# Optimization experiments

Measured on AMD Instinct MI355X. Metric: run time of the kernel, lower is better.

## Reference

```python
import jax, jax.numpy as jnp
import numpy as np

TOPK = 32
NUM_PT = 8192
NUM_KP = 8
HW = 19200


def _conv3(x, w, b):
    # x: [1, C, N], w: [O, C, 3] -> [1, O, N] (padding=1)
    y = jax.lax.conv_general_dilated(x, w, (1,), [(1, 1)],
                                     dimension_numbers=('NCH', 'OIH', 'NCH'))
    return y + b[None, :, None]


def setup_inputs() -> dict:
    key = jax.random.key(0)
    ks = jax.random.split(key, 64)

    def p(i, *shape):
        return (jax.random.normal(ks[i], shape, dtype=jnp.float32) * 0.05)

    inp = {
        'seg': jax.random.uniform(ks[0], (1, NUM_PT), dtype=jnp.float32),
        'img': jax.random.normal(ks[1], (1, 32, HW), dtype=jnp.float32),
        'cloud': jax.random.normal(ks[2], (1, NUM_PT, 3), dtype=jnp.float32),
        't': jax.random.normal(ks[3], (1, 3), dtype=jnp.float32),
        'choose': jax.random.randint(ks[4], (1, 1, NUM_PT), 0, HW),
        # Pseudo3DConv params (all 1x1 conv1d == channel matmul)
        'pconv1_w': p(5, 64, 3),    'pconv1_b': p(6, 64),
        'pconv2_w': p(7, 128, 64),  'pconv2_b': p(8, 128),
        'conv1_w': p(9, 64, 32),    'conv1_b': p(10, 64),
        'conv2_w': p(11, 128, 64),  'conv2_b': p(12, 128),
        'psconv1_w': p(13, 256, 128), 'psconv1_b': p(14, 256),
        'psconv2_w': p(15, 128, 256), 'psconv2_b': p(16, 128),
        'final_w': p(17, 128, 416), 'final_b': p(18, 128),
        # heads
        'seg1_w': p(19, 64, 128, 3), 'seg1_b': p(20, 64),
        'seg2_w': p(21, 32, 64),     'seg2_b': p(22, 32),
        'seg3_w': p(23, 1, 32),      'seg3_b': p(24, 1),
        'dis1_w': p(25, 64, 128, 3), 'dis1_b': p(26, 64),
        'dis2_w': p(27, 32, 64),     'dis2_b': p(28, 32),
        'dis3_w': p(29, 1, 32),      'dis3_b': p(30, 1),
        'lin1_w': p(31, 90, 128),    'lin1_b': p(32, 90),
        'lin2_w': p(33, 64, 90),     'lin2_b': p(34, 64),
        'lin3_w': p(35, 3 * NUM_KP, 64), 'lin3_b': p(36, 3 * NUM_KP),
    }
    return inp


def reference(seg, img, cloud, t, choose,
              pconv1_w, pconv1_b, pconv2_w, pconv2_b,
              conv1_w, conv1_b, conv2_w, conv2_b,
              psconv1_w, psconv1_b, psconv2_w, psconv2_b,
              final_w, final_b,
              seg1_w, seg1_b, seg2_w, seg2_b, seg3_w, seg3_b,
              dis1_w, dis1_b, dis2_w, dis2_b, dis3_w, dis3_b,
              lin1_w, lin1_b, lin2_w, lin2_b, lin3_w, lin3_b):
    lrelu = jax.nn.leaky_relu  # slope 0.01, same as torch default
    N = NUM_PT

    # gather per-point image features at chosen pixels: [N, 32]
    feat = jnp.take(img[0], choose[0, 0], axis=1).T
    c = cloud[0]  # [N, 3]

    # ---- KNN (self included, as in knn_cuda) ----
    d2 = jnp.sum((c[:, None, :] - c[None, :, :]) ** 2, axis=-1)  # [N, N]
    _, idx = jax.lax.top_k(-d2, TOPK)  # [N, K] nearest neighbors

    # ---- point-feature MLP (pconv1 -> lrelu -> pconv2) ----
    pf = lrelu(c @ pconv1_w.T + pconv1_b) @ pconv2_w.T + pconv2_b  # [N, 128]

    # ---- vectorized per-point neighbor gather + MLP + weighted maxpool ----
    nf = feat[idx]    # [N, K, 32]
    npf = pf[idx]     # [N, K, 128]
    npos = c[idx]     # [N, K, 3]
    w = jax.nn.softmax(-jnp.linalg.norm(c[:, None, :] - npos, axis=-1), axis=1)  # [N, K]

    f = lrelu(nf @ conv1_w.T + conv1_b) @ conv2_w.T + conv2_b          # [N, K, 128]
    fp = lrelu(npf @ psconv1_w.T + psconv1_b) @ psconv2_w.T + psconv2_b  # [N, K, 128]
    f = jnp.max(f * w[..., None], axis=1)    # [N, 128]
    fp = jnp.max(fp * w[..., None], axis=1)  # [N, 128]

    # final2 = [fp | img_feat], final1 = [f | cloud_feat] -> cat -> [N, 416]
    final = jnp.concatenate([fp, feat, f, pf], axis=1)
    fused = lrelu(final) @ final_w.T + final_b  # [N, 128]
    fused = fused.T[None]  # [1, 128, N]

    def pw(x, w_, b_):  # 1x1 conv1d on [1, C, N]
        return jnp.einsum('oc,bcn->bon', w_, x) + b_[None, :, None]

    # segmentation head
    h = lrelu(_conv3(fused, seg1_w, seg1_b))
    seg_pre = pw(lrelu(pw(h, seg2_w, seg2_b)), seg3_w, seg3_b).reshape(1, N)

    # distance-to-center weighting (norm along coord dim, softmax over points)
    dis_center = jax.nn.softmax(
        jnp.linalg.norm(cloud - (-t)[:, None, :], axis=2), axis=1)  # [1, N]

    # distance head (on unweighted fused features, matching torch op order)
    h = lrelu(_conv3(fused, dis1_w, dis1_b))
    dis_pre = pw(lrelu(pw(h, dis2_w, dis2_b)), dis3_w, dis3_b).reshape(1, N)

    # weight fused features by center distance and segmentation, sum-pool
    fused = fused * dis_center[:, None, :] * seg[:, None, :]
    g = jnp.sum(fused, axis=2)  # [1, 128]

    kp = lrelu(g @ lin1_w.T + lin1_b)
    kp = lrelu(kp @ lin2_w.T + lin2_b)
    keypoints = (kp @ lin3_w.T + lin3_b).reshape(1, NUM_KP, 3)
    return keypoints, dis_pre, dis_center, seg_pre
```

## Files before the change

kernel.cpp:

```cpp
#include <hip/hip_runtime.h>
#include <math.h>

#define NPT 8192
#define HWIMG 19200
#define KCAP 128

using short8 = __attribute__((ext_vector_type(8))) short;
using short4v = __attribute__((ext_vector_type(4))) short;
using f32x4  = __attribute__((ext_vector_type(4))) float;

__device__ __forceinline__ float lrelu(float x) { return x > 0.f ? x : 0.01f * x; }
__device__ __forceinline__ unsigned short f2bf(float v) {
  unsigned u = __float_as_uint(v);
  return (unsigned short)((u + 0x7fffu + ((u >> 16) & 1u)) >> 16);
}
__device__ __forceinline__ float bf2f(unsigned short h) {
  return __uint_as_float(((unsigned)h) << 16);
}
__device__ __forceinline__ void split2(float v, unsigned short& h, unsigned short& l) {
  h = f2bf(v);
  l = f2bf(v - bf2f(h));
}
__device__ __forceinline__ void mfma3(f32x4& acc, short8 ah, short8 al, short8 wh, short8 wl) {
  acc = __builtin_amdgcn_mfma_f32_16x16x32_bf16(ah, wh, acc, 0, 0, 0);
  acc = __builtin_amdgcn_mfma_f32_16x16x32_bf16(al, wh, acc, 0, 0, 0);
  acc = __builtin_amdgcn_mfma_f32_16x16x32_bf16(ah, wl, acc, 0, 0, 0);
}

__device__ __forceinline__ int swz(int o, int k, int Kc) {
  return ((((o >> 4) * Kc + (k >> 5)) << 6) + (((k >> 3) & 3) << 4) + (o & 15)) * 8 + (k & 7);
}

#define OFF_PCONV2  0
#define OFF_CONV1   8192
#define OFF_CONV2   10240
#define OFF_PSCONV1 18432
#define OFF_PSCONV2 51200
#define OFF_FINAL   83968
#define OFF_W3      137216
#define OFF_W2P     186368

#define S_C4    NPT
#define S_G     129
#define S_BIASC 128
#define S_B2C   64
#define S_FEAT  (NPT*32)
#define S_W3    49152
#define S_W2P   8192
#define S_WSPL  OFF_W3
#define PREP_TOTAL (S_C4 + S_G + S_BIASC + S_B2C + S_FEAT + S_W3 + S_W2P + S_WSPL)
__global__ void k_prep(const float* __restrict__ cloud, const int* __restrict__ choose,
                       const float* __restrict__ img,
                       const float* __restrict__ seg1_w, const float* __restrict__ dis1_w,
                       const float* __restrict__ seg1_b, const float* __restrict__ dis1_b,
                       const float* __restrict__ seg2_w, const float* __restrict__ dis2_w,
                       const float* __restrict__ seg2_b, const float* __restrict__ dis2_b,
                       const float* __restrict__ pconv2_w, const float* __restrict__ conv1_w,
                       const float* __restrict__ conv2_w, const float* __restrict__ psconv1_w,
                       const float* __restrict__ psconv2_w, const float* __restrict__ final_w,
                       float* __restrict__ c4, float* __restrict__ g,
                       float* __restrict__ biasc, float* __restrict__ bias2c,
                       float* __restrict__ feat,
                       unsigned short* __restrict__ feat_h, unsigned short* __restrict__ feat_l,
                       unsigned short* __restrict__ Wh, unsigned short* __restrict__ Wl) {
  int j = blockIdx.x * blockDim.x + threadIdx.x;
  if (j < S_C4) {
    float x = cloud[j*3+0], y = cloud[j*3+1], z = cloud[j*3+2];
    float4 v; v.x = x; v.y = y; v.z = z; v.w = x*x + y*y + z*z;
    ((float4*)c4)[j] = v;
    return;
  }
  j -= S_C4;
  if (j < S_G) { g[j] = 0.f; return; }
  j -= S_G;
  if (j < S_BIASC) { biasc[j] = (j < 64) ? seg1_b[j] : dis1_b[j-64]; return; }
  j -= S_BIASC;
  if (j < S_B2C) { bias2c[j] = (j < 32) ? seg2_b[j] : dis2_b[j-32]; return; }
  j -= S_B2C;
  if (j < S_FEAT) {
    int n = j >> 5, ch = j & 31;
    float v = img[ch*HWIMG + choose[n]];
    feat[j] = v;
    unsigned short hh, ll; split2(v, hh, ll);
    int d = swz(n, ch, 1);
    feat_h[d] = hh; feat_l[d] = ll;
    return;
  }
  j -= S_FEAT;
  if (j < S_W3) {
    int h = j / 24576, r = j - h*24576, o = r / 384, k = r - o*384;
    int t = k >> 7, c = k & 127;
    float v = (h ? dis1_w : seg1_w)[o*384 + c*3 + t];
    unsigned short hh, ll; split2(v, hh, ll);
    int d = OFF_W3 + swz(h*64 + o, k, 12);
    Wh[d] = hh; Wl[d] = ll;
    return;
  }
  j -= S_W3;
  if (j < S_W2P) {
    int o = j >> 7, c = j & 127;
    float v = 0.f;
    if (o < 32) { if (c < 64) v = seg2_w[o*64 + c]; }
    else        { if (c >= 64) v = dis2_w[(o-32)*64 + (c-64)]; }
    unsigned short hh, ll; split2(v, hh, ll);
    int d = OFF_W2P + swz(o, c, 4);
    Wh[d] = hh; Wl[d] = ll;
    return;
  }
  j -= S_W2P;
  if (j < S_WSPL) {
    float v; int d;
    if (j < OFF_CONV1) {
      int o = j >> 6, k = j & 63;
      v = pconv2_w[j]; d = OFF_PCONV2 + swz(o, k, 2);
    } else if (j < OFF_CONV2) {
      int jj = j - OFF_CONV1, o = jj >> 5, k = jj & 31;
      v = conv1_w[jj]; d = OFF_CONV1 + swz(o, k, 1);
    } else if (j < OFF_PSCONV1) {
      int jj = j - OFF_CONV2, o = jj >> 6, k = jj & 63;
      v = conv2_w[jj]; d = OFF_CONV2 + swz(o, k, 2);
    } else if (j < OFF_PSCONV2) {
      int jj = j - OFF_PSCONV1, o = jj >> 7, k = jj & 127;
      v = psconv1_w[jj]; d = OFF_PSCONV1 + swz(o, k, 4);
    } else if (j < OFF_FINAL) {
      int jj = j - OFF_PSCONV2, o = jj >> 8, k = jj & 255;
      v = psconv2_w[jj]; d = OFF_PSCONV2 + swz(o, k, 8);
    } else {
      int jj = j - OFF_FINAL, o = jj / 416, k = jj - o*416;
      v = final_w[jj]; d = OFF_FINAL + swz(o, k, 13);
    }
    unsigned short hh, ll; split2(v, hh, ll);
    Wh[d] = hh; Wl[d] = ll;
  }
}

__device__ __forceinline__ unsigned bsort32u(unsigned key, int lane) {
#pragma unroll
  for (int k = 2; k <= 64; k <<= 1) {
#pragma unroll
    for (int j = k >> 1; j > 0; j >>= 1) {
      unsigned o = __shfl_xor(key, j, 64);
      bool keepmin = (((lane & j) == 0) == ((lane & k) == 0));
      key = ((o < key) == keepmin) ? o : key;
    }
  }
  return key;
}
__device__ __forceinline__ unsigned long long bsort64(unsigned long long key, int lane) {
#pragma unroll
  for (int k = 2; k <= 64; k <<= 1) {
#pragma unroll
    for (int j = k >> 1; j > 0; j >>= 1) {
      unsigned long long o = __shfl_xor(key, j, 64);
      bool keepmin = (((lane & j) == 0) == ((lane & k) == 0));
      bool omin = o < key;
      key = (omin == keepmin) ? o : key;
    }
  }
  return key;
}
__device__ __forceinline__ unsigned long long bmerge64(unsigned long long key, int lane) {
#pragma unroll
  for (int j = 32; j > 0; j >>= 1) {
    unsigned long long o = __shfl_xor(key, j, 64);
    bool keepmin = ((lane & j) == 0);
    bool omin = o < key;
    key = (omin == keepmin) ? o : key;
  }
  return key;
}

#define MEGA_GRID 3073
__global__ __launch_bounds__(256) void k_mega(const float4* __restrict__ c4,
                                              int* __restrict__ idxo, float* __restrict__ wo,
                                              const float* __restrict__ cloud,
                                              const float* __restrict__ tvec,
                                              float* __restrict__ dc,
                                              const float* __restrict__ pconv1_w, const float* __restrict__ pconv1_b,
                                              const float* __restrict__ pconv2_b, const float* __restrict__ psconv1_b,
                                              const float* __restrict__ psconv2_b,
                                              const unsigned short* __restrict__ feat_h,
                                              const unsigned short* __restrict__ feat_l,
                                              const float* __restrict__ conv1_b, const float* __restrict__ conv2_b,
                                              const unsigned short* __restrict__ Wh,
                                              const unsigned short* __restrict__ Wl,
                                              float* __restrict__ pf, float* __restrict__ Yfp,
                                              float* __restrict__ Yf) {
  __shared__ __align__(16) char smem[16384];
  int tid = threadIdx.x, lane = tid & 63, w = tid >> 6;
  int mr = lane & 15, q = lane >> 4;
  if (blockIdx.x > 2048) {
    unsigned short* sh_h = (unsigned short*)smem;
    unsigned short* sh_l = (unsigned short*)(smem + 8192);
    int cb = blockIdx.x - 2049;
    if (cb < 512) {
      int m0 = cb * 16;
      float4 cp = c4[m0 + mr];
      short8 ah0, al0, ah1, al1;
#pragma unroll
      for (int j = 0; j < 8; ++j) {
        int c0 = q*8 + j, c1 = 32 + q*8 + j;
        float v0 = lrelu(fmaf(cp.x, pconv1_w[c0*3+0], fmaf(cp.y, pconv1_w[c0*3+1],
                          fmaf(cp.z, pconv1_w[c0*3+2], pconv1_b[c0]))));
        float v1 = lrelu(fmaf(cp.x, pconv1_w[c1*3+0], fmaf(cp.y, pconv1_w[c1*3+1],
                          fmaf(cp.z, pconv1_w[c1*3+2], pconv1_b[c1]))));
        unsigned short hh, ll;
        split2(v0, hh, ll); ah0[j] = (short)hh; al0[j] = (short)ll;
        split2(v1, hh, ll); ah1[j] = (short)hh; al1[j] = (short)ll;
      }
      f32x4 acc[2];
#pragma unroll
      for (int t = 0; t < 2; ++t) { f32x4 z = {0.f,0.f,0.f,0.f}; acc[t] = z; }
      const unsigned short* W2h = Wh + OFF_PCONV2;
      const unsigned short* W2l = Wl + OFF_PCONV2;
#pragma unroll
      for (int tt = 0; tt < 2; ++tt) {
        int t1 = 2*w + tt;
        int w0 = ((t1*2 + 0)*64 + lane)*8, w1 = ((t1*2 + 1)*64 + lane)*8;
        mfma3(acc[tt], ah0, al0, *(const short8*)(W2h + w0), *(const short8*)(W2l + w0));
        mfma3(acc[tt], ah1, al1, *(const short8*)(W2h + w1), *(const short8*)(W2l + w1));
      }
#pragma unroll
      for (int tt = 0; tt < 2; ++tt) {
        int t1 = 2*w + tt, n = t1*16 + mr;
        float b = pconv2_b[n];
        int ks2 = t1 >> 1, q2 = (t1 & 1)*2 + (mr >> 3), jd = mr & 7;
#pragma unroll
        for (int r = 0; r < 4; ++r) {
          int row = q*4 + r;
          float v = acc[tt][r] + b;
          pf[(size_t)(m0+row)*128 + n] = v;
          unsigned short hh, ll; split2(v, hh, ll);
          int p = ((ks2*16 + row)*4 + q2)*8 + jd;
          sh_h[p] = hh; sh_l[p] = ll;
        }
      }
      __syncthreads();
      f32x4 acc3[2];
#pragma unroll
      for (int t = 0; t < 2; ++t) { f32x4 z = {0.f,0.f,0.f,0.f}; acc3[t] = z; }
      const unsigned short* W3h = Wh + OFF_PSCONV1;
      const unsigned short* W3l = Wl + OFF_PSCONV1;
      const unsigned short* W4h = Wh + OFF_PSCONV2;
      const unsigned short* W4l = Wl + OFF_PSCONV2;
#pragma unroll
      for (int h = 0; h < 2; ++h) {
        f32x4 acc2[2];
#pragma unroll
        for (int t = 0; t < 2; ++t) { f32x4 z = {0.f,0.f,0.f,0.f}; acc2[t] = z; }
#pragma unroll
        for (int ks = 0; ks < 4; ++ks) {
          int ap = ((ks*16 + mr)*4 + q)*8;
          short8 ah = *(const short8*)&sh_h[ap];
          short8 al = *(const short8*)&sh_l[ap];
#pragma unroll
          for (int tt = 0; tt < 2; ++tt) {
            int ts = h*8 + 2*w + tt;
            int wb = ((ts*4 + ks)*64 + lane)*8;
            mfma3(acc2[tt], ah, al, *(const short8*)(W3h + wb), *(const short8*)(W3l + wb));
          }
        }
#pragma unroll
        for (int tt = 0; tt < 2; ++tt) {
          int tl = 2*w + tt;
          int n = h*128 + tl*16 + mr;
          float b = psconv1_b[n];
          int ks3 = tl >> 1, q3 = (tl & 1)*2 + (mr >> 3), jd = mr & 7;
#pragma unroll
          for (int r = 0; r < 4; ++r) {
            int row = q*4 + r;
            float v = lrelu(acc2[tt][r] + b);
            unsigned short hh, ll; split2(v, hh, ll);
            int p = 2048 + ((ks3*16 + row)*4 + q3)*8 + jd;
            sh_h[p] = hh; sh_l[p] = ll;
          }
        }
        __syncthreads();
#pragma unroll
        for (int ks = 0; ks < 4; ++ks) {
          int ap = 2048 + ((ks*16 + mr)*4 + q)*8;
          short8 ah = *(const short8*)&sh_h[ap];
          short8 al = *(const short8*)&sh_l[ap];
#pragma unroll
          for (int tt = 0; tt < 2; ++tt) {
            int wb = (((2*w+tt)*8 + h*4 + ks)*64 + lane)*8;
            mfma3(acc3[tt], ah, al, *(const short8*)(W4h + wb), *(const short8*)(W4l + wb));
          }
        }
        __syncthreads();
      }
#pragma unroll
      for (int tt = 0; tt < 2; ++tt) {
        int n = (2*w+tt)*16 + mr;
        float b = psconv2_b[n];
#pragma unroll
        for (int r = 0; r < 4; ++r)
          Yfp[(size_t)(m0 + q*4 + r)*128 + n] = acc3[tt][r] + b;
      }
    } else {
      int m0 = (cb - 512) * 16;
      int ab = ((m0 >> 4)*64 + lane)*8;
      short8 ah = *(const short8*)(feat_h + ab);
      short8 al = *(const short8*)(feat_l + ab);
      f32x4 acc = {0.f,0.f,0.f,0.f};
      const unsigned short* W1h = Wh + OFF_CONV1;
      const unsigned short* W1l = Wl + OFF_CONV1;
      {
        int wb = (w*64 + lane)*8;
        mfma3(acc, ah, al, *(const short8*)(W1h + wb), *(const short8*)(W1l + wb));
      }
      {
        int n = w*16 + mr;
        float b = conv1_b[n];
        int ks2 = n >> 5, q2 = (n >> 3) & 3, jd = mr & 7;
#pragma unroll
        for (int r = 0; r < 4; ++r) {
          int row = q*4 + r;
          float v = lrelu(acc[r] + b);
          unsigned short hh, ll; split2(v, hh, ll);
          int p = ((ks2*16 + row)*4 + q2)*8 + jd;
          sh_h[p] = hh; sh_l[p] = ll;
        }
      }
      __syncthreads();
      f32x4 acc2[2];
#pragma unroll
      for (int t = 0; t < 2; ++t) { f32x4 z = {0.f,0.f,0.f,0.f}; acc2[t] = z; }
      const unsigned short* W2h = Wh + OFF_CONV2;
      const unsigned short* W2l = Wl + OFF_CONV2;
#pragma unroll
      for (int ks = 0; ks < 2; ++ks) {
        int ap = ((ks*16 + mr)*4 + q)*8;
        short8 a2 = *(const short8*)&sh_h[ap];
        short8 a2l = *(const short8*)&sh_l[ap];
#pragma unroll
        for (int tt = 0; tt < 2; ++tt) {
          int wb = (((2*w+tt)*2 + ks)*64 + lane)*8;
          mfma3(acc2[tt], a2, a2l, *(const short8*)(W2h + wb), *(const short8*)(W2l + wb));
        }
      }
#pragma unroll
      for (int tt = 0; tt < 2; ++tt) {
        int n = (2*w+tt)*16 + mr;
        float b = conv2_b[n];
#pragma unroll
        for (int r = 0; r < 4; ++r)
          Yf[(size_t)(m0 + q*4 + r)*128 + n] = acc2[tt][r] + b;
      }
    }
    return;
  }
  if (blockIdx.x == 2048) {
    float* sred = (float*)smem;
    float tx = tvec[0], ty = tvec[1], tz = tvec[2];
    float v[32];
    float m = -INFINITY;
#pragma unroll
    for (int i2 = 0; i2 < 32; ++i2) {
      int n = i2*256 + tid;
      float ax = cloud[n*3+0] + tx, ay = cloud[n*3+1] + ty, az = cloud[n*3+2] + tz;
      v[i2] = sqrtf(ax*ax + ay*ay + az*az);
      m = fmaxf(m, v[i2]);
    }
#pragma unroll
    for (int o = 1; o < 64; o <<= 1) m = fmaxf(m, __shfl_xor(m, o, 64));
    if (lane == 0) sred[w] = m;
    __syncthreads();
    m = fmaxf(fmaxf(sred[0], sred[1]), fmaxf(sred[2], sred[3]));
    __syncthreads();
    float s = 0.f;
#pragma unroll
    for (int i2 = 0; i2 < 32; ++i2) { v[i2] = expf(v[i2] - m); s += v[i2]; }
#pragma unroll
    for (int o = 1; o < 64; o <<= 1) s += __shfl_xor(s, o, 64);
    if (lane == 0) sred[w] = s;
    __syncthreads();
    s = sred[0] + sred[1] + sred[2] + sred[3];
#pragma unroll
    for (int i2 = 0; i2 < 32; ++i2) dc[i2*256 + tid] = v[i2] / s;
    return;
  }
  float (*smin)[256] = (float(*)[256])smem;
  float* sTv = (float*)(smem + 4096);
  int*   scnt = (int*)(smem + 4112);
  float (*sd)[KCAP] = (float(*)[KCAP])(smem + 4128);
  int   (*sj)[KCAP] = (int(*)[KCAP])(smem + 6176);
  int q0 = blockIdx.x * 4;
  float4 p0 = c4[q0], p1 = c4[q0+1], p2 = c4[q0+2], p3 = c4[q0+3];
  float p0x = -2.f*p0.x, p0y = -2.f*p0.y, p0z = -2.f*p0.z;
  float p1x = -2.f*p1.x, p1y = -2.f*p1.y, p1z = -2.f*p1.z;
  float p2x = -2.f*p2.x, p2y = -2.f*p2.y, p2z = -2.f*p2.z;
  float p3x = -2.f*p3.x, p3y = -2.f*p3.y, p3z = -2.f*p3.z;
#define DDOT(PX,PY,PZ,PW,CJ) fmaf(PX,(CJ).x, fmaf(PY,(CJ).y, fmaf(PZ,(CJ).z, PW + (CJ).w)))
  float m0 = INFINITY, m1 = INFINITY, m2 = INFINITY, m3 = INFINITY;
  for (int t = 0; t < 32; ++t) {
    float4 cj = c4[t*256 + tid];
    m0 = fminf(m0, DDOT(p0x,p0y,p0z,p0.w,cj));
    m1 = fminf(m1, DDOT(p1x,p1y,p1z,p1.w,cj));
    m2 = fminf(m2, DDOT(p2x,p2y,p2z,p2.w,cj));
    m3 = fminf(m3, DDOT(p3x,p3y,p3z,p3.w,cj));
  }
  smin[0][tid] = m0; smin[1][tid] = m1; smin[2][tid] = m2; smin[3][tid] = m3;
  if (tid < 4) scnt[tid] = 0;
  __syncthreads();
  {
    float4 vv = *(const float4*)&smin[w][lane*4];
    float m4 = fmaxf(fminf(fminf(vv.x, vv.y), fminf(vv.z, vv.w)), 0.f);
    unsigned key = bsort32u(__float_as_uint(m4), lane);
    float T = __uint_as_float(__shfl(key, 31, 64));
    if (lane == 0) sTv[w] = T * (1.f + 2e-5f) + 4e-5f;
  }
  __syncthreads();
  float T0 = sTv[0], T1 = sTv[1], T2 = sTv[2], T3 = sTv[3];
  for (int t = 0; t < 32; ++t) {
    int j = t*256 + tid;
    float4 cj = c4[j];
    float d;
#define APPEND(Q, P) { \
    float dx_ = (P).x-cj.x, dy_ = (P).y-cj.y, dz_ = (P).z-cj.z; \
    float de_ = dx_*dx_ + dy_*dy_ + dz_*dz_; \
    int p_ = atomicAdd(&scnt[Q],1); if (p_ < KCAP) { sd[Q][p_] = de_; sj[Q][p_] = j; } }
    d = DDOT(p0x,p0y,p0z,p0.w,cj); if (d <= T0) APPEND(0, p0);
    d = DDOT(p1x,p1y,p1z,p1.w,cj); if (d <= T1) APPEND(1, p1);
    d = DDOT(p2x,p2y,p2z,p2.w,cj); if (d <= T2) APPEND(2, p2);
    d = DDOT(p3x,p3y,p3z,p3.w,cj); if (d <= T3) APPEND(3, p3);
  }
  __syncthreads();
  int M = scnt[w]; if (M > KCAP) M = KCAP;
  unsigned long long key = (lane < M)
      ? (((unsigned long long)__float_as_uint(sd[w][lane]) << 32) | (unsigned)sj[w][lane])
      : ~0ull;
  key = bsort64(key, lane);
  for (int base = 64; base < M; base += 64) {
    unsigned long long nk = (base + lane < M)
        ? (((unsigned long long)__float_as_uint(sd[w][base+lane]) << 32) | (unsigned)sj[w][base+lane])
        : ~0ull;
    nk = bsort64(nk, lane);
    nk = __shfl_xor(nk, 63, 64);
    key = key < nk ? key : nk;
    key = bmerge64(key, lane);
  }
  float dsel = __uint_as_float((unsigned)(key >> 32));
  int   jsel = (int)(unsigned)(key & 0xffffffffu);
  float v = -sqrtf(dsel);
  float mx = v;
#pragma unroll
  for (int o = 1; o < 32; o <<= 1) mx = fmaxf(mx, __shfl_xor(mx, o, 64));
  float e = expf(v - mx);
  float s = e;
#pragma unroll
  for (int o = 1; o < 32; o <<= 1) s += __shfl_xor(s, o, 64);
  if (lane < 32) {
    int qd = q0 + w;
    wo[qd*32 + lane] = e / s;
    idxo[qd*32 + lane] = jsel;
  }
}

__global__ __launch_bounds__(256) void k_tail(const float* __restrict__ Yf,
                                              const float* __restrict__ Yfp,
                                              const float* __restrict__ feat,
                                              const float* __restrict__ pf,
                                              const int* __restrict__ idx,
                                              const float* __restrict__ wsm,
                                              const unsigned short* __restrict__ Wh,
                                              const unsigned short* __restrict__ Wl,
                                              const float* __restrict__ final_b,
                                              const float* __restrict__ biasc,
                                              const float* __restrict__ bias2c,
                                              const float* __restrict__ segw, const float* __restrict__ segb,
                                              const float* __restrict__ disw, const float* __restrict__ disb,
                                              unsigned short* __restrict__ fusedh,
                                              unsigned short* __restrict__ fusedl,
                                              float* __restrict__ osegp, float* __restrict__ odisp) {
  __shared__ int sjn[18][32];
  __shared__ float swn[18][32];
  __shared__ __align__(16) char sbuf[37440];
  int tid = threadIdx.x, lane = tid & 63, w = tid >> 6;
  int mr = lane & 15, q = lane >> 4;
  int mt = blockIdx.x, m0 = mt * 16;
  for (int t = tid; t < 18*32; t += 256) {
    int lr = t >> 5, k = t & 31, gr = m0 - 1 + lr;
    if (gr >= 0 && gr < NPT) { sjn[lr][k] = idx[gr*32+k]; swn[lr][k] = wsm[gr*32+k]; }
    else { sjn[lr][k] = 0; swn[lr][k] = 0.f; }
  }
  __syncthreads();
  for (int t = tid; t < 1872; t += 256) {
    int lr, col;
    float4 v4;
    if (t < 1152) {
      lr = t >> 6; int arr = (t >> 5) & 1, cg = t & 31;
      const float* Y = arr ? Yf : Yfp;
      float ax = -INFINITY, ay = -INFINITY, az = -INFINITY, aw = -INFINITY;
#pragma unroll 8
      for (int k = 0; k < 32; ++k) {
        float4 vv = *(const float4*)&Y[(size_t)sjn[lr][k]*128 + cg*4];
        float wk = swn[lr][k];
        ax = fmaxf(ax, wk*vv.x); ay = fmaxf(ay, wk*vv.y);
        az = fmaxf(az, wk*vv.z); aw = fmaxf(aw, wk*vv.w);
      }
      v4.x = lrelu(ax); v4.y = lrelu(ay); v4.z = lrelu(az); v4.w = lrelu(aw);
      col = (arr ? 160 : 0) + cg*4;
    } else if (t < 1728) {
      int u = t - 1152; lr = u >> 5; int cg = u & 31;
      int gr = m0 - 1 + lr;
      int gc = gr < 0 ? 0 : (gr >= NPT ? NPT-1 : gr);
      float4 p4 = *(const float4*)&pf[(size_t)gc*128 + cg*4];
      v4.x = lrelu(p4.x); v4.y = lrelu(p4.y); v4.z = lrelu(p4.z); v4.w = lrelu(p4.w);
      col = 288 + cg*4;
    } else {
      int u = t - 1728; lr = u >> 3; int cg = u & 7;
      int gr = m0 - 1 + lr;
      int gc = gr < 0 ? 0 : (gr >= NPT ? NPT-1 : gr);
      float4 p4 = *(const float4*)&feat[(size_t)gc*32 + cg*4];
      v4.x = lrelu(p4.x); v4.y = lrelu(p4.y); v4.z = lrelu(p4.z); v4.w = lrelu(p4.w);
      col = 128 + cg*4;
    }
    int gr = m0 - 1 + lr;
    if (gr < 0 || gr >= NPT) { v4.x = 0.f; v4.y = 0.f; v4.z = 0.f; v4.w = 0.f; }
    int ks = col >> 5, qq = (col >> 3) & 3, j0 = col & 7;
    char* base = sbuf + (ks*18 + lr)*80 + qq*16 + j0*2;
    short4v hv, lv;
    unsigned short hh, ll;
    split2(v4.x, hh, ll); hv[0] = (short)hh; lv[0] = (short)ll;
    split2(v4.y, hh, ll); hv[1] = (short)hh; lv[1] = (short)ll;
    split2(v4.z, hh, ll); hv[2] = (short)hh; lv[2] = (short)ll;
    split2(v4.w, hh, ll); hv[3] = (short)hh; lv[3] = (short)ll;
    *(short4v*)base = hv;
    *(short4v*)(base + 18720) = lv;
  }
  __syncthreads();
  f32x4 accA[2], accB[2];
#pragma unroll
  for (int t = 0; t < 2; ++t) {
    f32x4 z = {0.f,0.f,0.f,0.f}; accA[t] = z; accB[t] = z;
  }
  const unsigned short* WFh = Wh + OFF_FINAL;
  const unsigned short* WFl = Wl + OFF_FINAL;
#pragma unroll
  for (int ks = 0; ks < 13; ++ks) {
    int arB = 16 + mr; if (arB > 17) arB = 17;
    const char* pA = sbuf + (ks*18 + mr)*80 + q*16;
    const char* pB = sbuf + (ks*18 + arB)*80 + q*16;
    short8 ahA = *(const short8*)pA;
    short8 alA = *(const short8*)(pA + 18720);
    short8 ahB = *(const short8*)pB;
    short8 alB = *(const short8*)(pB + 18720);
#pragma unroll
    for (int tt = 0; tt < 2; ++tt) {
      int wb = (((2*w+tt)*13 + ks)*64 + lane)*8;
      short8 wh = *(const short8*)(WFh + wb);
      short8 wl = *(const short8*)(WFl + wb);
      mfma3(accA[tt], ahA, alA, wh, wl);
      mfma3(accB[tt], ahB, alB, wh, wl);
    }
  }
  __syncthreads();
#pragma unroll
  for (int tile = 0; tile < 2; ++tile) {
#pragma unroll
    for (int tt = 0; tt < 2; ++tt) {
      int t2 = 2*w + tt, n = t2*16 + mr;
      float b = final_b[n];
      int ksA = t2 >> 1, qq = (t2 & 1)*2 + (mr >> 3), jd = mr & 7;
#pragma unroll
      for (int r = 0; r < 4; ++r) {
        int lr = tile*16 + q*4 + r;
        if (lr > 17) continue;
        int gr = m0 - 1 + lr;
        float v = (tile ? accB[tt][r] : accA[tt][r]) + b;
        if (gr < 0 || gr >= NPT) v = 0.f;
        unsigned short hh, ll; split2(v, hh, ll);
        char* p = sbuf + (ksA*18 + lr)*80 + qq*16 + jd*2;
        *(unsigned short*)p = hh;
        *(unsigned short*)(p + 5760) = ll;
      }
    }
  }
  __syncthreads();
  {
    int ks2 = tid >> 6, q2 = (tid >> 4) & 3, mr2 = tid & 15;
    int lr = mr2 + 1;
    const char* p = sbuf + (ks2*18 + lr)*80 + q2*16;
    short8 oh = *(const short8*)p;
    short8 ol = *(const short8*)(p + 5760);
    size_t pos = ((size_t)mt*256 + tid)*8;
    *(short8*)(fusedh + pos) = oh;
    *(short8*)(fusedl + pos) = ol;
  }
  f32x4 acc3[2];
#pragma unroll
  for (int t = 0; t < 2; ++t) { f32x4 z = {0.f,0.f,0.f,0.f}; acc3[t] = z; }
  const unsigned short* W3h = Wh + OFF_W3;
  const unsigned short* W3l = Wl + OFF_W3;
#pragma unroll
  for (int ks = 0; ks < 12; ++ks) {
    int tap = ks >> 2, ksA = ks & 3;
    int ar = mr + tap;
    const char* p = sbuf + (ksA*18 + ar)*80 + q*16;
    short8 ah = *(const short8*)p;
    short8 al = *(const short8*)(p + 5760);
#pragma unroll
    for (int tt = 0; tt < 2; ++tt) {
      int wb = (((2*w+tt)*12 + ks)*64 + lane)*8;
      mfma3(acc3[tt], ah, al, *(const short8*)(W3h + wb), *(const short8*)(W3l + wb));
    }
  }
#pragma unroll
  for (int tt = 0; tt < 2; ++tt) {
    int t2 = 2*w + tt, n = t2*16 + mr;
    float b = biasc[n];
    int ks2 = t2 >> 1, q2 = (t2 & 1)*2 + (mr >> 3), jd = mr & 7;
#pragma unroll
    for (int r = 0; r < 4; ++r) {
      int row = q*4 + r;
      float v = lrelu(acc3[tt][r] + b);
      unsigned short hh, ll; split2(v, hh, ll);
      char* p = sbuf + 11520 + (ks2*16 + row)*80 + q2*16 + jd*2;
      *(unsigned short*)p = hh;
      *(unsigned short*)(p + 5120) = ll;
    }
  }
  __syncthreads();
  f32x4 acc4 = {0.f,0.f,0.f,0.f};
  const unsigned short* WPh = Wh + OFF_W2P;
  const unsigned short* WPl = Wl + OFF_W2P;
#pragma unroll
  for (int ks = 0; ks < 4; ++ks) {
    const char* p = sbuf + 11520 + (ks*16 + mr)*80 + q*16;
    short8 ah = *(const short8*)p;
    short8 al = *(const short8*)(p + 5120);
    int wb = ((w*4 + ks)*64 + lane)*8;
    mfma3(acc4, ah, al, *(const short8*)(WPh + wb), *(const short8*)(WPl + wb));
  }
  float hw = (w < 2) ? segw[w*16 + mr] : disw[(w-2)*16 + mr];
  float bb = bias2c[w*16 + mr];
  float* shead = (float*)(sbuf + 21760);
#pragma unroll
  for (int r = 0; r < 4; ++r)
    shead[(w*16 + q*4 + r)*17 + mr] = lrelu(acc4[r] + bb) * hw;
  __syncthreads();
  if (tid < 16) {
    float a = 0.f;
#pragma unroll
    for (int i = 0; i < 16; ++i) a += shead[(tid)*17 + i] + shead[(16 + tid)*17 + i];
    osegp[m0 + tid] = a + segb[0];
  } else if (tid < 32) {
    int r2 = tid - 16;
    float a = 0.f;
#pragma unroll
    for (int i = 0; i < 16; ++i) a += shead[(32 + r2)*17 + i] + shead[(48 + r2)*17 + i];
    odisp[m0 + r2] = a + disb[0];
  }
}

__global__ __launch_bounds__(256) void k_gk(const unsigned short* __restrict__ Ah,
                                            const unsigned short* __restrict__ Al,
                                            const float* __restrict__ dc,
                                            const float* __restrict__ seg,
                                            float* __restrict__ g,
                                            const float* __restrict__ l1w, const float* __restrict__ l1b,
                                            const float* __restrict__ l2w, const float* __restrict__ l2b,
                                            const float* __restrict__ l3w, const float* __restrict__ l3b,
                                            float* __restrict__ o_kp) {
  __shared__ float sred[2048];
  __shared__ int slast;
  int tid = threadIdx.x;
  int b = blockIdx.x;
  float pg[8] = {0.f,0.f,0.f,0.f,0.f,0.f,0.f,0.f};
  int mrr = tid & 15;
  for (int mi = 0; mi < 16; ++mi) {
    int m = b*16 + mi;
    int row = m*16 + mrr;
    float wrow = dc[row] * seg[row];
    size_t pos = ((size_t)m*256 + tid)*8;
    short8 hv = *(const short8*)(Ah + pos);
    short8 lv = *(const short8*)(Al + pos);
#pragma unroll
    for (int j = 0; j < 8; ++j)
      pg[j] += (bf2f((unsigned short)hv[j]) + bf2f((unsigned short)lv[j])) * wrow;
  }
#pragma unroll
  for (int j = 0; j < 8; ++j) sred[tid*8 + j] = pg[j];
  __syncthreads();
  if (tid < 128) {
    int ks = tid >> 5, q2 = (tid >> 3) & 3, j = tid & 7;
    float s = 0.f;
#pragma unroll
    for (int mr2 = 0; mr2 < 16; ++mr2) s += sred[((ks<<6) + (q2<<4) + mr2)*8 + j];
    atomicAdd(&g[tid], s);
  }
  __threadfence();
  __syncthreads();
  if (tid == 0) slast = (atomicAdd((int*)(g + 128), 1) == 31);
  __syncthreads();
  if (!slast) return;
  __shared__ float sg[128], s1[90], s2[64];
  if (tid < 128) sg[tid] = atomicAdd(&g[tid], 0.f);
  __syncthreads();
  if (tid < 90) {
    float a = l1b[tid];
    for (int i = 0; i < 128; ++i) a += sg[i]*l1w[tid*128+i];
    s1[tid] = lrelu(a);
  }
  __syncthreads();
  if (tid < 64) {
    float a = l2b[tid];
    for (int i = 0; i < 90; ++i) a += s1[i]*l2w[tid*90+i];
    s2[tid] = lrelu(a);
  }
  __syncthreads();
  if (tid < 24) {
    float a = l3b[tid];
    for (int i = 0; i < 64; ++i) a += s2[i]*l3w[tid*64+i];
    o_kp[tid] = a;
  }
}

extern "C" void kernel_launch(void* const* d_in, const int* in_sizes, int n_in,
                              void* d_out, int out_size, void* d_ws, size_t ws_size,
                              hipStream_t stream) {
  const float* seg      = (const float*)d_in[0];
  const float* img      = (const float*)d_in[1];
  const float* cloud    = (const float*)d_in[2];
  const float* tvec     = (const float*)d_in[3];
  const int*   choose   = (const int*)d_in[4];
  const float* pconv1_w = (const float*)d_in[5];
  const float* pconv1_b = (const float*)d_in[6];
  const float* pconv2_w = (const float*)d_in[7];
  const float* pconv2_b = (const float*)d_in[8];
  const float* conv1_w  = (const float*)d_in[9];
  const float* conv1_b  = (const float*)d_in[10];
  const float* conv2_w  = (const float*)d_in[11];
  const float* conv2_b  = (const float*)d_in[12];
  const float* psconv1_w= (const float*)d_in[13];
  const float* psconv1_b= (const float*)d_in[14];
  const float* psconv2_w= (const float*)d_in[15];
  const float* psconv2_b= (const float*)d_in[16];
  const float* final_w  = (const float*)d_in[17];
  const float* final_b  = (const float*)d_in[18];
  const float* seg1_w   = (const float*)d_in[19];
  const float* seg1_b   = (const float*)d_in[20];
  const float* seg2_w   = (const float*)d_in[21];
  const float* seg2_b   = (const float*)d_in[22];
  const float* seg3_w   = (const float*)d_in[23];
  const float* seg3_b   = (const float*)d_in[24];
  const float* dis1_w   = (const float*)d_in[25];
  const float* dis1_b   = (const float*)d_in[26];
  const float* dis2_w   = (const float*)d_in[27];
  const float* dis2_b   = (const float*)d_in[28];
  const float* dis3_w   = (const float*)d_in[29];
  const float* dis3_b   = (const float*)d_in[30];
  const float* lin1_w   = (const float*)d_in[31];
  const float* lin1_b   = (const float*)d_in[32];
  const float* lin2_w   = (const float*)d_in[33];
  const float* lin2_b   = (const float*)d_in[34];
  const float* lin3_w   = (const float*)d_in[35];
  const float* lin3_b   = (const float*)d_in[36];

  float* out = (float*)d_out;
  float* ws  = (float*)d_ws;

  float* c4     = ws + 0;
  float* feat   = ws + 32768;
  unsigned short* feat_h = (unsigned short*)(ws + 294912);
  unsigned short* feat_l = (unsigned short*)(ws + 425984);
  float* pf     = ws + 557056;
  float* Yf     = ws + 1605632;
  float* Yfp    = ws + 2654208;
  int*   idx    = (int*)(ws + 3702784);
  float* wsm    = ws + 3964928;
  unsigned short* fusedh = (unsigned short*)(ws + 8683520);
  unsigned short* fusedl = (unsigned short*)(ws + 9207808);
  unsigned short* Wh    = (unsigned short*)(ws + 9732096);
  unsigned short* Wl    = (unsigned short*)(ws + 9829376);
  float* biasc  = ws + 9926656;
  float* bias2c = ws + 9926784;
  float* g      = ws + 9926848;

  float* o_kp   = out;
  float* o_disp = out + 24;
  float* o_dc   = out + 8216;
  float* o_segp = out + 16408;

  k_prep<<<(PREP_TOTAL + 255)/256, 256, 0, stream>>>(
      cloud, choose, img, seg1_w, dis1_w, seg1_b, dis1_b,
      seg2_w, dis2_w, seg2_b, dis2_b,
      pconv2_w, conv1_w, conv2_w, psconv1_w, psconv2_w, final_w,
      c4, g, biasc, bias2c, feat, feat_h, feat_l, Wh, Wl);

  k_mega<<<MEGA_GRID, 256, 0, stream>>>(
      (const float4*)c4, idx, wsm, cloud, tvec, o_dc,
      pconv1_w, pconv1_b, pconv2_b, psconv1_b, psconv2_b,
      feat_h, feat_l, conv1_b, conv2_b, Wh, Wl, pf, Yfp, Yf);

  k_tail<<<512, 256, 0, stream>>>(
      Yf, Yfp, feat, pf, idx, wsm, Wh, Wl,
      final_b, biasc, bias2c, seg3_w, seg3_b, dis3_w, dis3_b,
      fusedh, fusedl, o_segp, o_disp);

  k_gk<<<32, 256, 0, stream>>>(fusedh, fusedl, o_dc, seg, g,
                               lin1_w, lin1_b, lin2_w, lin2_b, lin3_w, lin3_b, o_kp);

  (void)in_sizes; (void)n_in; (void)out_size; (void)ws_size;
}
```

Measured before the change: 232.5 us.

## Fuse weighted pooling and keypoint MLP into tail kernel; unroll kNN scans

Removes the separate pooling/keypoint kernel. The tail kernel now computes the center-distance and segmentation weighted sum of its fused features directly from shared memory and atomically accumulates them into the global vector. The last finishing block then runs the small MLP. This removes the round trip of the split-precision fused activations to global memory and one kernel launch. The cost is 512 blocks doing global atomics instead of 32. Separately, the kNN min-scan and append loops are unrolled by two to put more independent loads in flight.

```diff
diff --git a/kernel.cpp b/kernel.cpp
--- a/kernel.cpp
+++ b/kernel.cpp
@@ -393,12 +393,17 @@
   float p3x = -2.f*p3.x, p3y = -2.f*p3.y, p3z = -2.f*p3.z;
 #define DDOT(PX,PY,PZ,PW,CJ) fmaf(PX,(CJ).x, fmaf(PY,(CJ).y, fmaf(PZ,(CJ).z, PW + (CJ).w)))
   float m0 = INFINITY, m1 = INFINITY, m2 = INFINITY, m3 = INFINITY;
-  for (int t = 0; t < 32; ++t) {
-    float4 cj = c4[t*256 + tid];
-    m0 = fminf(m0, DDOT(p0x,p0y,p0z,p0.w,cj));
-    m1 = fminf(m1, DDOT(p1x,p1y,p1z,p1.w,cj));
-    m2 = fminf(m2, DDOT(p2x,p2y,p2z,p2.w,cj));
-    m3 = fminf(m3, DDOT(p3x,p3y,p3z,p3.w,cj));
+  for (int t = 0; t < 32; t += 2) {
+    float4 ca = c4[t*256 + tid];
+    float4 cb = c4[t*256 + 256 + tid];
+    float a0 = DDOT(p0x,p0y,p0z,p0.w,ca), b0 = DDOT(p0x,p0y,p0z,p0.w,cb);
+    float a1 = DDOT(p1x,p1y,p1z,p1.w,ca), b1 = DDOT(p1x,p1y,p1z,p1.w,cb);
+    float a2 = DDOT(p2x,p2y,p2z,p2.w,ca), b2 = DDOT(p2x,p2y,p2z,p2.w,cb);
+    float a3 = DDOT(p3x,p3y,p3z,p3.w,ca), b3 = DDOT(p3x,p3y,p3z,p3.w,cb);
+    m0 = fminf(m0, fminf(a0, b0));
+    m1 = fminf(m1, fminf(a1, b1));
+    m2 = fminf(m2, fminf(a2, b2));
+    m3 = fminf(m3, fminf(a3, b3));
   }
   smin[0][tid] = m0; smin[1][tid] = m1; smin[2][tid] = m2; smin[3][tid] = m3;
   if (tid < 4) scnt[tid] = 0;
@@ -412,18 +417,23 @@
   }
   __syncthreads();
   float T0 = sTv[0], T1 = sTv[1], T2 = sTv[2], T3 = sTv[3];
-  for (int t = 0; t < 32; ++t) {
-    int j = t*256 + tid;
-    float4 cj = c4[j];
+#define APPEND(Q, P, CJ, J) { \
+    float dx_ = (P).x-(CJ).x, dy_ = (P).y-(CJ).y, dz_ = (P).z-(CJ).z; \
+    float de_ = dx_*dx_ + dy_*dy_ + dz_*dz_; \
+    int p_ = atomicAdd(&scnt[Q],1); if (p_ < KCAP) { sd[Q][p_] = de_; sj[Q][p_] = (J); } }
+  for (int t = 0; t < 32; t += 2) {
+    int ja = t*256 + tid, jb = ja + 256;
+    float4 ca = c4[ja];
+    float4 cb = c4[jb];
     float d;
-#define APPEND(Q, P) { \
-    float dx_ = (P).x-cj.x, dy_ = (P).y-cj.y, dz_ = (P).z-cj.z; \
-    float de_ = dx_*dx_ + dy_*dy_ + dz_*dz_; \
-    int p_ = atomicAdd(&scnt[Q],1); if (p_ < KCAP) { sd[Q][p_] = de_; sj[Q][p_] = j; } }
-    d = DDOT(p0x,p0y,p0z,p0.w,cj); if (d <= T0) APPEND(0, p0);
-    d = DDOT(p1x,p1y,p1z,p1.w,cj); if (d <= T1) APPEND(1, p1);
-    d = DDOT(p2x,p2y,p2z,p2.w,cj); if (d <= T2) APPEND(2, p2);
-    d = DDOT(p3x,p3y,p3z,p3.w,cj); if (d <= T3) APPEND(3, p3);
+    d = DDOT(p0x,p0y,p0z,p0.w,ca); if (d <= T0) APPEND(0, p0, ca, ja);
+    d = DDOT(p1x,p1y,p1z,p1.w,ca); if (d <= T1) APPEND(1, p1, ca, ja);
+    d = DDOT(p2x,p2y,p2z,p2.w,ca); if (d <= T2) APPEND(2, p2, ca, ja);
+    d = DDOT(p3x,p3y,p3z,p3.w,ca); if (d <= T3) APPEND(3, p3, ca, ja);
+    d = DDOT(p0x,p0y,p0z,p0.w,cb); if (d <= T0) APPEND(0, p0, cb, jb);
+    d = DDOT(p1x,p1y,p1z,p1.w,cb); if (d <= T1) APPEND(1, p1, cb, jb);
+    d = DDOT(p2x,p2y,p2z,p2.w,cb); if (d <= T2) APPEND(2, p2, cb, jb);
+    d = DDOT(p3x,p3y,p3z,p3.w,cb); if (d <= T3) APPEND(3, p3, cb, jb);
   }
   __syncthreads();
   int M = scnt[w]; if (M > KCAP) M = KCAP;
@@ -470,11 +480,16 @@
                                               const float* __restrict__ bias2c,
                                               const float* __restrict__ segw, const float* __restrict__ segb,
                                               const float* __restrict__ disw, const float* __restrict__ disb,
-                                              unsigned short* __restrict__ fusedh,
-                                              unsigned short* __restrict__ fusedl,
-                                              float* __restrict__ osegp, float* __restrict__ odisp) {
+                                              const float* __restrict__ dcw, const float* __restrict__ segin,
+                                              float* __restrict__ g,
+                                              const float* __restrict__ l1w, const float* __restrict__ l1b,
+                                              const float* __restrict__ l2w, const float* __restrict__ l2b,
+                                              const float* __restrict__ l3w, const float* __restrict__ l3b,
+                                              float* __restrict__ osegp, float* __restrict__ odisp,
+                                              float* __restrict__ o_kp) {
   __shared__ int sjn[18][32];
   __shared__ float swn[18][32];
+  __shared__ int slast;
   __shared__ __align__(16) char sbuf[37440];
   int tid = threadIdx.x, lane = tid & 63, w = tid >> 6;
   int mr = lane & 15, q = lane >> 4;
@@ -584,9 +599,21 @@
     const char* p = sbuf + (ks2*18 + lr)*80 + q2*16;
     short8 oh = *(const short8*)p;
     short8 ol = *(const short8*)(p + 5760);
-    size_t pos = ((size_t)mt*256 + tid)*8;
-    *(short8*)(fusedh + pos) = oh;
-    *(short8*)(fusedl + pos) = ol;
+    int gr = m0 + mr2;
+    float wrow = dcw[gr] * segin[gr];
+    float* sred = (float*)(sbuf + 26112);
+#pragma unroll
+    for (int j = 0; j < 8; ++j)
+      sred[tid*8 + j] = (bf2f((unsigned short)oh[j]) + bf2f((unsigned short)ol[j])) * wrow;
+  }
+  __syncthreads();
+  if (tid < 128) {
+    float* sred = (float*)(sbuf + 26112);
+    int ks = tid >> 5, q2 = (tid >> 3) & 3, j = tid & 7;
+    float s = 0.f;
+#pragma unroll
+    for (int mr2 = 0; mr2 < 16; ++mr2) s += sred[((ks << 6) + (q2 << 4) + mr2)*8 + j];
+    atomicAdd(&g[tid], s);
   }
   f32x4 acc3[2];
 #pragma unroll
@@ -652,50 +679,14 @@
     for (int i = 0; i < 16; ++i) a += shead[(32 + r2)*17 + i] + shead[(48 + r2)*17 + i];
     odisp[m0 + r2] = a + disb[0];
   }
-}
-
-__global__ __launch_bounds__(256) void k_gk(const unsigned short* __restrict__ Ah,
-                                            const unsigned short* __restrict__ Al,
-                                            const float* __restrict__ dc,
-                                            const float* __restrict__ seg,
-                                            float* __restrict__ g,
-                                            const float* __restrict__ l1w, const float* __restrict__ l1b,
-                                            const float* __restrict__ l2w, const float* __restrict__ l2b,
-                                            const float* __restrict__ l3w, const float* __restrict__ l3b,
-                                            float* __restrict__ o_kp) {
-  __shared__ float sred[2048];
-  __shared__ int slast;
-  int tid = threadIdx.x;
-  int b = blockIdx.x;
-  float pg[8] = {0.f,0.f,0.f,0.f,0.f,0.f,0.f,0.f};
-  int mrr = tid & 15;
-  for (int mi = 0; mi < 16; ++mi) {
-    int m = b*16 + mi;
-    int row = m*16 + mrr;
-    float wrow = dc[row] * seg[row];
-    size_t pos = ((size_t)m*256 + tid)*8;
-    short8 hv = *(const short8*)(Ah + pos);
-    short8 lv = *(const short8*)(Al + pos);
-#pragma unroll
-    for (int j = 0; j < 8; ++j)
-      pg[j] += (bf2f((unsigned short)hv[j]) + bf2f((unsigned short)lv[j])) * wrow;
-  }
-#pragma unroll
-  for (int j = 0; j < 8; ++j) sred[tid*8 + j] = pg[j];
-  __syncthreads();
-  if (tid < 128) {
-    int ks = tid >> 5, q2 = (tid >> 3) & 3, j = tid & 7;
-    float s = 0.f;
-#pragma unroll
-    for (int mr2 = 0; mr2 < 16; ++mr2) s += sred[((ks<<6) + (q2<<4) + mr2)*8 + j];
-    atomicAdd(&g[tid], s);
-  }
   __threadfence();
   __syncthreads();
-  if (tid == 0) slast = (atomicAdd((int*)(g + 128), 1) == 31);
+  if (tid == 0) slast = (atomicAdd((int*)(g + 128), 1) == 511);
   __syncthreads();
   if (!slast) return;
-  __shared__ float sg[128], s1[90], s2[64];
+  float* sg = (float*)(sbuf + 26112);
+  float* s1 = sg + 128;
+  float* s2 = s1 + 90;
   if (tid < 128) sg[tid] = atomicAdd(&g[tid], 0.f);
   __syncthreads();
   if (tid < 90) {
@@ -770,8 +761,6 @@
   float* Yfp    = ws + 2654208;
   int*   idx    = (int*)(ws + 3702784);
   float* wsm    = ws + 3964928;
-  unsigned short* fusedh = (unsigned short*)(ws + 8683520);
-  unsigned short* fusedl = (unsigned short*)(ws + 9207808);
   unsigned short* Wh    = (unsigned short*)(ws + 9732096);
   unsigned short* Wl    = (unsigned short*)(ws + 9829376);
   float* biasc  = ws + 9926656;
@@ -797,10 +786,9 @@
   k_tail<<<512, 256, 0, stream>>>(
       Yf, Yfp, feat, pf, idx, wsm, Wh, Wl,
       final_b, biasc, bias2c, seg3_w, seg3_b, dis3_w, dis3_b,
-      fusedh, fusedl, o_segp, o_disp);
-
-  k_gk<<<32, 256, 0, stream>>>(fusedh, fusedl, o_dc, seg, g,
-                               lin1_w, lin1_b, lin2_w, lin2_b, lin3_w, lin3_b, o_kp);
+      o_dc, seg, g,
+      lin1_w, lin1_b, lin2_w, lin2_b, lin3_w, lin3_b,
+      o_segp, o_disp, o_kp);
 
   (void)in_sizes; (void)n_in; (void)out_size; (void)ws_size;
 }
```

Result: slower. 262.3 us (+12.8%).
